# Optimization experiments

Hardware: AMD Instinct MI355X
Metric: run time of the kernel (lower is better)

Reference implementation:

```python
import jax, jax.numpy as jnp
import numpy as np

EMBED = 1024
HEADS = 16


def setup_inputs() -> dict:
    key = jax.random.key(0)
    ks = jax.random.split(key, 7)
    scale = 1.0 / np.sqrt(EMBED)
    x = jax.random.normal(ks[0], (4, 2048, EMBED), dtype=jnp.float32)
    Wq = jax.random.normal(ks[1], (EMBED, EMBED), dtype=jnp.float32) * scale
    bq = jax.random.normal(ks[2], (EMBED,), dtype=jnp.float32) * 0.01
    Wk = jax.random.normal(ks[3], (EMBED, EMBED), dtype=jnp.float32) * scale
    bk = jax.random.normal(ks[4], (EMBED,), dtype=jnp.float32) * 0.01
    Wv = jax.random.normal(ks[5], (EMBED, EMBED), dtype=jnp.float32) * scale
    bv = jax.random.normal(ks[6], (EMBED,), dtype=jnp.float32) * 0.01
    return {"x": x, "Wq": Wq, "bq": bq, "Wk": Wk, "bk": bk, "Wv": Wv, "bv": bv}


def reference(x, Wq, bq, Wk, bk, Wv, bv):
    b, s, n = x.shape
    h = HEADS
    d = n // h
    # torch nn.Linear: y = x @ W.T + b
    q = (jnp.einsum("bsn,mn->bsm", x, Wq) + bq).reshape(b, s, h, d).transpose(0, 2, 1, 3)
    k = (jnp.einsum("bsn,mn->bsm", x, Wk) + bk).reshape(b, s, h, d).transpose(0, 2, 1, 3)
    v = (jnp.einsum("bsn,mn->bsm", x, Wv) + bv).reshape(b, s, h, d).transpose(0, 2, 1, 3)
    # scores: [b, h, s_q, s_k]; fixed scale of 1/10 as in the source
    scores = jnp.einsum("bhqd,bhkd->bhqk", q, k) / 10.0
    # NOTE: softmax over dim=-2 (the QUERY axis), matching the source exactly
    attn = jax.nn.softmax(scores, axis=-2)
    out = jnp.einsum("bhqk,bhkd->bhqd", attn, v)
    return out.transpose(0, 2, 1, 3).reshape(b, s, n)
```

## Files before the change

### kernel.cpp

```cpp
#include <hip/hip_runtime.h>
#include <math.h>

#define SEQ    2048
#define EMBED  1024
#define HEADS  16
#define HDIM   64
#define BATCH  4
#define ROWS   (BATCH * SEQ)
#define BH     (BATCH * HEADS)

typedef _Float16 f16;
typedef __attribute__((ext_vector_type(8))) _Float16 f16x8;
typedef __attribute__((ext_vector_type(4))) _Float16 f16x4;
typedef __attribute__((ext_vector_type(4))) float    f32x4;

#define LOG2E_10 0.14426950408889634f

__device__ __forceinline__ float fast_exp2(float x) { return __builtin_amdgcn_exp2f(x); }

__device__ __forceinline__ void async16(void* l, const void* g) {
    __builtin_amdgcn_global_load_lds(
        (__attribute__((address_space(1))) void*)(uintptr_t)g,
        (__attribute__((address_space(3))) void*)(uint32_t)(uintptr_t)l,
        16, 0, 0);
}

__device__ __forceinline__ f32x4 mfma16(f16x8 a, f16x8 b, f32x4 c) {
    return __builtin_amdgcn_mfma_f32_16x16x32_f16(a, b, c, 0, 0, 0);
}
__device__ __forceinline__ f32x4 mfma16k16(f16x4 a, f16x4 b, f32x4 c) {
    return __builtin_amdgcn_mfma_f32_16x16x16f16(a, b, c, 0, 0, 0);
}

#define NX4 (ROWS * EMBED / 4)
#define NW4 (EMBED * EMBED / 4)
__global__ __launch_bounds__(256) void cvt_kernel(
    const float* __restrict__ x,
    const float* __restrict__ Wq, const float* __restrict__ Wk,
    const float* __restrict__ Wv,
    f16* __restrict__ xh, f16* __restrict__ Wh)
{
    int i = blockIdx.x * 256 + threadIdx.x;
    const float4* src; f16* dst; int j;
    if (i < NX4)              { src = (const float4*)x;  dst = xh;                j = i; }
    else if (i < NX4 + NW4)   { src = (const float4*)Wq; dst = Wh;                j = i - NX4; }
    else if (i < NX4 + 2*NW4) { src = (const float4*)Wk; dst = Wh + EMBED*EMBED;  j = i - NX4 - NW4; }
    else                      { src = (const float4*)Wv; dst = Wh + 2*EMBED*EMBED;j = i - NX4 - 2*NW4; }
    float4 v = src[j];
    f16x4 h;
    h[0] = (f16)v.x; h[1] = (f16)v.y; h[2] = (f16)v.z; h[3] = (f16)v.w;
    *(f16x4*)(dst + (size_t)j * 4) = h;
}

__global__ __launch_bounds__(256) void proj_kernel(
    const f16* __restrict__ A,
    const f16* __restrict__ W,
    const float* __restrict__ bq, const float* __restrict__ bk,
    const float* __restrict__ bv,
    f16* __restrict__ Qh, f16* __restrict__ Kh, f16* __restrict__ Vt)
{
    __shared__ f16 As[128 * 32];
    __shared__ f16 Bs[128 * 32];

    const int t = threadIdx.x, wv = t >> 6, lane = t & 63;
    const int lm = lane & 15, quad = lane >> 4;
    const int r0 = blockIdx.x * 128, c0 = blockIdx.y * 128;
    const int wm = wv & 1, wn = wv >> 1;

    const int srow = wv * 32 + (lane >> 2);
    const int sch  = (lane & 3) * 8;
    const f16* gA = A + (size_t)(r0 + srow) * EMBED + sch;
    const f16* gB = W + (size_t)(c0 + srow) * EMBED + sch;
    f16* lA = As + wv * 1024;
    f16* lB = Bs + wv * 1024;

    f32x4 acc[4][4];
#pragma unroll
    for (int i = 0; i < 4; ++i)
#pragma unroll
        for (int j = 0; j < 4; ++j) acc[i][j] = (f32x4){0.f, 0.f, 0.f, 0.f};

    for (int kk = 0; kk < EMBED; kk += 32) {
        __syncthreads();
        async16(lA,        gA + kk);
        async16(lA + 512,  gA + 16 * EMBED + kk);
        async16(lB,        gB + kk);
        async16(lB + 512,  gB + 16 * EMBED + kk);
        __syncthreads();

        f16x8 af[4], bf[4];
#pragma unroll
        for (int i = 0; i < 4; ++i)
            af[i] = *(const f16x8*)&As[(wm * 64 + i * 16 + lm) * 32 + quad * 8];
#pragma unroll
        for (int i = 0; i < 4; ++i)
            bf[i] = *(const f16x8*)&Bs[(wn * 64 + i * 16 + lm) * 32 + quad * 8];
#pragma unroll
        for (int mi = 0; mi < 4; ++mi)
#pragma unroll
            for (int ni = 0; ni < 4; ++ni)
                acc[mi][ni] = mfma16(af[mi], bf[ni], acc[mi][ni]);
    }

    const int z = c0 >> 10;
    const float* bias = (z == 0) ? bq : (z == 1) ? bk : bv;
    const float osc = (z == 0) ? LOG2E_10 : 1.0f;
#pragma unroll
    for (int ni = 0; ni < 4; ++ni) {
        int col = c0 + wn * 64 + ni * 16 + lm;
        int cz  = col & 1023;
        float bb = bias[cz];
        int h = cz >> 6, d = cz & 63;
#pragma unroll
        for (int mi = 0; mi < 4; ++mi) {
            int rbase = r0 + wm * 64 + mi * 16 + quad * 4;
            int b = rbase >> 11, s = rbase & 2047;
            if (z < 2) {
                f16* O = (z == 0) ? Qh : Kh;
                size_t base = ((size_t)(b * HEADS + h) * SEQ + s) * HDIM + d;
#pragma unroll
                for (int r = 0; r < 4; ++r)
                    O[base + (size_t)r * HDIM] = (f16)((acc[mi][ni][r] + bb) * osc);
            } else {
                f16x4 pk;
#pragma unroll
                for (int r = 0; r < 4; ++r) pk[r] = (f16)(acc[mi][ni][r] + bb);
                *(f16x4*)&Vt[((size_t)(b * HEADS + h) * HDIM + d) * SEQ + s] = pk;
            }
        }
    }
}

__device__ __forceinline__ void xcd_decode(int d, int& bh, int& x128) {
    int xcd  = d & 7;
    int r    = d >> 3;
    x128     = (r & 15) * 128;
    bh       = (r >> 4) * 8 + xcd;
}

__global__ __launch_bounds__(256) void stats_kernel(
    const f16* __restrict__ Qh, const f16* __restrict__ Kh,
    const f16* __restrict__ Vt, f16* __restrict__ Vt2)
{
    __shared__ f16 Ks[128 * 64];
    __shared__ f16 Qs[64 * 64];

    const int t = threadIdx.x, wv = t >> 6, lane = t & 63;
    const int lm = lane & 15, quad = lane >> 4;
    int bh, k0;
    xcd_decode(blockIdx.x, bh, k0);
    const int grow = lane >> 3;
    const int gsw  = ((lane & 7) ^ grow) * 8;
    const int rs   = lm & 7;
    const size_t base = (size_t)bh * SEQ * HDIM;

#pragma unroll
    for (int i = 0; i < 4; ++i) {
        int g = wv * 4 + i;
        async16(Ks + g * 512, Kh + base + (size_t)(k0 + g * 8 + grow) * HDIM + gsw);
    }
    __syncthreads();

    f16x8 kf[2][2];
#pragma unroll
    for (int ct = 0; ct < 2; ++ct)
#pragma unroll
        for (int ds = 0; ds < 2; ++ds)
            kf[ct][ds] = *(const f16x8*)&Ks[(wv * 32 + ct * 16 + lm) * 64
                                            + (((ds * 4 + quad) ^ rs) << 3)];

    float cs0 = 0.f, cs1 = 0.f;
    for (int q0 = 0; q0 < SEQ; q0 += 64) {
        __syncthreads();
#pragma unroll
        for (int i = 0; i < 2; ++i) {
            int g = wv * 2 + i;
            async16(Qs + g * 512, Qh + base + (size_t)(q0 + g * 8 + grow) * HDIM + gsw);
        }
        __syncthreads();
#pragma unroll
        for (int qt = 0; qt < 4; ++qt) {
            f16x8 a0 = *(const f16x8*)&Qs[(qt * 16 + lm) * 64 + ((quad ^ rs) << 3)];
            f16x8 a1 = *(const f16x8*)&Qs[(qt * 16 + lm) * 64 + (((4 + quad) ^ rs) << 3)];
            f32x4 c0v = (f32x4){0.f, 0.f, 0.f, 0.f};
            f32x4 c1v = (f32x4){0.f, 0.f, 0.f, 0.f};
            c0v = mfma16(a0, kf[0][0], c0v); c0v = mfma16(a1, kf[0][1], c0v);
            c1v = mfma16(a0, kf[1][0], c1v); c1v = mfma16(a1, kf[1][1], c1v);
#pragma unroll
            for (int r = 0; r < 4; ++r) {
                cs0 += fast_exp2(c0v[r]);
                cs1 += fast_exp2(c1v[r]);
            }
        }
    }
    cs0 += __shfl_xor(cs0, 16, 64); cs0 += __shfl_xor(cs0, 32, 64);
    cs1 += __shfl_xor(cs1, 16, 64); cs1 += __shfl_xor(cs1, 32, 64);

    __syncthreads();
    float* sc = (float*)Qs;
    if (quad == 0) {
        sc[wv * 32 + lm]      = 1024.0f / cs0;
        sc[wv * 32 + 16 + lm] = 1024.0f / cs1;
    }
    __syncthreads();
    const int row = t >> 2, cb = (t & 3) * 32;
    const f16* src = Vt  + base + (size_t)row * SEQ + k0 + cb;
    f16*       dst = Vt2 + base + (size_t)row * SEQ + k0 + cb;
#pragma unroll
    for (int c = 0; c < 4; ++c) {
        f16x8 v = *(const f16x8*)(src + c * 8);
        f16x8 o;
#pragma unroll
        for (int j = 0; j < 8; ++j)
            o[j] = (f16)((float)v[j] * sc[cb + c * 8 + j]);
        *(f16x8*)(dst + c * 8) = o;
    }
}

__global__ __launch_bounds__(256) void out_kernel(
    const f16* __restrict__ Qh, const f16* __restrict__ Kh,
    const f16* __restrict__ Vt2, float* __restrict__ out)
{
    __shared__ f16 L[16384];

    const int t = threadIdx.x, wv = t >> 6, lane = t & 63;
    const int lm = lane & 15, quad = lane >> 4;
    const int wq = wv >> 1, wk = wv & 1;
    int bh, q0;
    xcd_decode(blockIdx.x, bh, q0);
    const int b = bh >> 4, h = bh & 15;
    const int grow = lane >> 3;
    const int gsw  = ((lane & 7) ^ grow) * 8;
    const int rs   = lm & 7;
    const size_t base = (size_t)bh * SEQ * HDIM;

    f16* Ks = L;
    f16* Vs = L + 8192;

    f16x8 qa[4][2];
#pragma unroll
    for (int qt = 0; qt < 4; ++qt)
#pragma unroll
        for (int ds = 0; ds < 2; ++ds)
            qa[qt][ds] = *(const f16x8*)(Qh + base
                          + (size_t)(q0 + wq * 64 + qt * 16 + lm) * HDIM
                          + ds * 32 + quad * 8);

#pragma unroll
    for (int i = 0; i < 2; ++i) {
        int g = wv * 2 + i;
        async16(Ks + g * 512, Kh  + base + (size_t)(g * 8 + grow) * HDIM + gsw);
        async16(Vs + g * 512, Vt2 + base + (size_t)(g * 8 + grow) * SEQ + gsw);
    }
    __syncthreads();

    f32x4 oacc[4][4];
#pragma unroll
    for (int i = 0; i < 4; ++i)
#pragma unroll
        for (int j = 0; j < 4; ++j) oacc[i][j] = (f32x4){0.f, 0.f, 0.f, 0.f};

    for (int it = 0; it < SEQ / 64; ++it) {
        const int cur = it & 1;
        if (it + 1 < SEQ / 64) {
            const int nxt = cur ^ 1, k0n = (it + 1) * 64;
#pragma unroll
            for (int i = 0; i < 2; ++i) {
                int g = wv * 2 + i;
                async16(Ks + nxt * 4096 + g * 512,
                        Kh + base + (size_t)(k0n + g * 8 + grow) * HDIM + gsw);
                async16(Vs + nxt * 4096 + g * 512,
                        Vt2 + base + (size_t)(g * 8 + grow) * SEQ + k0n + gsw);
            }
        }
        const f16* Kb = Ks + cur * 4096;
        const f16* Vb = Vs + cur * 4096;

#pragma unroll
        for (int ct = 0; ct < 2; ++ct) {
            const int kb = wk * 32 + ct * 16;
            f16x8 kf0 = *(const f16x8*)&Kb[(kb + lm) * 64 + ((quad ^ rs) << 3)];
            f16x8 kf1 = *(const f16x8*)&Kb[(kb + lm) * 64 + (((4 + quad) ^ rs) << 3)];
            const int vch = ((wk * 4 + ct * 2 + (quad >> 1)) ^ rs);
            f16x4 vb[4];
#pragma unroll
            for (int dt = 0; dt < 4; ++dt)
                vb[dt] = *(const f16x4*)&Vb[(dt * 16 + lm) * 64 + vch * 8 + (quad & 1) * 4];
#pragma unroll
            for (int qt = 0; qt < 4; ++qt) {
                f32x4 s4 = (f32x4){0.f, 0.f, 0.f, 0.f};
                s4 = mfma16(kf0, qa[qt][0], s4);
                s4 = mfma16(kf1, qa[qt][1], s4);
                f16x4 pa;
#pragma unroll
                for (int r = 0; r < 4; ++r)
                    pa[r] = (f16)fast_exp2(s4[r]);
#pragma unroll
                for (int dt = 0; dt < 4; ++dt)
                    oacc[qt][dt] = mfma16k16(pa, vb[dt], oacc[qt][dt]);
            }
        }
        __syncthreads();
    }

    float* red = (float*)L;
    if (wk == 1) {
#pragma unroll
        for (int qt = 0; qt < 4; ++qt)
#pragma unroll
            for (int dt = 0; dt < 4; ++dt)
#pragma unroll
                for (int r = 0; r < 4; ++r)
                    red[wq * 4096 + (qt * 16 + quad * 4 + r) * 64 + dt * 16 + lm]
                        = oacc[qt][dt][r];
    }
    __syncthreads();
    if (wk == 0) {
        const float inv1024 = 1.0f / 1024.0f;
#pragma unroll
        for (int qt = 0; qt < 4; ++qt)
#pragma unroll
            for (int dt = 0; dt < 4; ++dt) {
                int col = h * HDIM + dt * 16 + lm;
#pragma unroll
                for (int r = 0; r < 4; ++r) {
                    int ql = qt * 16 + quad * 4 + r;
                    int s  = q0 + wq * 64 + ql;
                    float v = oacc[qt][dt][r]
                            + red[wq * 4096 + ql * 64 + dt * 16 + lm];
                    out[((size_t)b * SEQ + s) * EMBED + col] = v * inv1024;
                }
            }
    }
}

extern "C" void kernel_launch(void* const* d_in, const int* in_sizes, int n_in,
                              void* d_out, int out_size, void* d_ws, size_t ws_size,
                              hipStream_t stream) {
    const float* x  = (const float*)d_in[0];
    const float* Wq = (const float*)d_in[1];
    const float* bq = (const float*)d_in[2];
    const float* Wk = (const float*)d_in[3];
    const float* bk = (const float*)d_in[4];
    const float* Wv = (const float*)d_in[5];
    const float* bv = (const float*)d_in[6];
    float* out = (float*)d_out;

    f16* xh = (f16*)d_ws;
    f16* Wh = xh + (size_t)ROWS * EMBED;
    f16* Qh = Wh + (size_t)3 * EMBED * EMBED;
    f16* Kh = Qh + (size_t)BH * SEQ * HDIM;
    f16* Vt = Kh + (size_t)BH * SEQ * HDIM;
    f16* Vt2 = xh;

    cvt_kernel<<<(NX4 + 3 * NW4) / 256, 256, 0, stream>>>(x, Wq, Wk, Wv, xh, Wh);
    proj_kernel<<<dim3(ROWS / 128, 3 * EMBED / 128), 256, 0, stream>>>(
        xh, Wh, bq, bk, bv, Qh, Kh, Vt);
    stats_kernel<<<dim3(SEQ / 128 * BH), 256, 0, stream>>>(Qh, Kh, Vt, Vt2);
    out_kernel<<<dim3(SEQ / 128 * BH), 256, 0, stream>>>(Qh, Kh, Vt2, out);
}
```

Before: 323.0 us.

## Prefetch two tiles ahead with explicit vmcnt waits in stats and out kernels

Both the stats and attention-output kernels now issue async global-to-LDS loads two tiles ahead into a double buffer. They replace __syncthreads with targeted s_waitcnt vmcnt/lgkmcnt waits plus raw barriers, so loads can stay in flight across iterations. The out kernel also stages its Q tile through LDS with the swizzled layout instead of direct strided global loads. The aim is to hide global memory latency behind MFMA and exp work, at the cost of fragile hand-counted wait values that assume a fixed number of outstanding loads per thread.

```diff
diff --git a/kernel.cpp b/kernel.cpp
--- a/kernel.cpp
+++ b/kernel.cpp
@@ -8,6 +8,7 @@
 #define BATCH  4
 #define ROWS   (BATCH * SEQ)
 #define BH     (BATCH * HEADS)
+#define NT     (SEQ / 64)
 
 typedef _Float16 f16;
 typedef __attribute__((ext_vector_type(8))) _Float16 f16x8;
@@ -17,6 +18,12 @@
 #define LOG2E_10 0.14426950408889634f
 
 __device__ __forceinline__ float fast_exp2(float x) { return __builtin_amdgcn_exp2f(x); }
+
+#define WAIT_VM0() asm volatile("s_waitcnt vmcnt(0)" ::: "memory")
+#define WAIT_VM2() asm volatile("s_waitcnt vmcnt(2)" ::: "memory")
+#define WAIT_VM4() asm volatile("s_waitcnt vmcnt(4)" ::: "memory")
+#define WAIT_LGKM0() asm volatile("s_waitcnt lgkmcnt(0)" ::: "memory")
+#define BAR() __builtin_amdgcn_s_barrier()
 
 __device__ __forceinline__ void async16(void* l, const void* g) {
     __builtin_amdgcn_global_load_lds(
@@ -143,7 +150,7 @@
     const f16* __restrict__ Vt, f16* __restrict__ Vt2)
 {
     __shared__ f16 Ks[128 * 64];
-    __shared__ f16 Qs[64 * 64];
+    __shared__ f16 Qs[2 * 64 * 64];
 
     const int t = threadIdx.x, wv = t >> 6, lane = t & 63;
     const int lm = lane & 15, quad = lane >> 4;
@@ -159,7 +166,16 @@
         int g = wv * 4 + i;
         async16(Ks + g * 512, Kh + base + (size_t)(k0 + g * 8 + grow) * HDIM + gsw);
     }
-    __syncthreads();
+#pragma unroll
+    for (int bi = 0; bi < 2; ++bi)
+#pragma unroll
+        for (int i = 0; i < 2; ++i) {
+            int g = wv * 2 + i;
+            async16(Qs + bi * 4096 + g * 512,
+                    Qh + base + (size_t)(bi * 64 + g * 8 + grow) * HDIM + gsw);
+        }
+    WAIT_VM4();
+    BAR();
 
     f16x8 kf[2][2];
 #pragma unroll
@@ -170,18 +186,15 @@
                                             + (((ds * 4 + quad) ^ rs) << 3)];
 
     float cs0 = 0.f, cs1 = 0.f;
-    for (int q0 = 0; q0 < SEQ; q0 += 64) {
-        __syncthreads();
-#pragma unroll
-        for (int i = 0; i < 2; ++i) {
-            int g = wv * 2 + i;
-            async16(Qs + g * 512, Qh + base + (size_t)(q0 + g * 8 + grow) * HDIM + gsw);
-        }
-        __syncthreads();
+    for (int it = 0; it < NT; ++it) {
+        const int cur = it & 1;
+        if (it == NT - 1) WAIT_VM0(); else WAIT_VM2();
+        BAR();
+        const f16* Qb = Qs + cur * 4096;
 #pragma unroll
         for (int qt = 0; qt < 4; ++qt) {
-            f16x8 a0 = *(const f16x8*)&Qs[(qt * 16 + lm) * 64 + ((quad ^ rs) << 3)];
-            f16x8 a1 = *(const f16x8*)&Qs[(qt * 16 + lm) * 64 + (((4 + quad) ^ rs) << 3)];
+            f16x8 a0 = *(const f16x8*)&Qb[(qt * 16 + lm) * 64 + ((quad ^ rs) << 3)];
+            f16x8 a1 = *(const f16x8*)&Qb[(qt * 16 + lm) * 64 + (((4 + quad) ^ rs) << 3)];
             f32x4 c0v = (f32x4){0.f, 0.f, 0.f, 0.f};
             f32x4 c1v = (f32x4){0.f, 0.f, 0.f, 0.f};
             c0v = mfma16(a0, kf[0][0], c0v); c0v = mfma16(a1, kf[0][1], c0v);
@@ -192,11 +205,21 @@
                 cs1 += fast_exp2(c1v[r]);
             }
         }
+        WAIT_LGKM0();
+        BAR();
+        if (it + 2 < NT) {
+            const int qn = (it + 2) * 64;
+#pragma unroll
+            for (int i = 0; i < 2; ++i) {
+                int g = wv * 2 + i;
+                async16(Qs + cur * 4096 + g * 512,
+                        Qh + base + (size_t)(qn + g * 8 + grow) * HDIM + gsw);
+            }
+        }
     }
     cs0 += __shfl_xor(cs0, 16, 64); cs0 += __shfl_xor(cs0, 32, 64);
     cs1 += __shfl_xor(cs1, 16, 64); cs1 += __shfl_xor(cs1, 32, 64);
 
-    __syncthreads();
     float* sc = (float*)Qs;
     if (quad == 0) {
         sc[wv * 32 + lm]      = 1024.0f / cs0;
@@ -234,25 +257,32 @@
     const int rs   = lm & 7;
     const size_t base = (size_t)bh * SEQ * HDIM;
 
-    f16* Ks = L;
-    f16* Vs = L + 8192;
-
+#pragma unroll
+    for (int i = 0; i < 4; ++i) {
+        int g = wv * 4 + i;
+        async16(L + g * 512, Qh + base + (size_t)(q0 + g * 8 + grow) * HDIM + gsw);
+    }
+    WAIT_VM0();
+    BAR();
     f16x8 qa[4][2];
 #pragma unroll
     for (int qt = 0; qt < 4; ++qt)
 #pragma unroll
         for (int ds = 0; ds < 2; ++ds)
-            qa[qt][ds] = *(const f16x8*)(Qh + base
-                          + (size_t)(q0 + wq * 64 + qt * 16 + lm) * HDIM
-                          + ds * 32 + quad * 8);
-
-#pragma unroll
-    for (int i = 0; i < 2; ++i) {
-        int g = wv * 2 + i;
-        async16(Ks + g * 512, Kh  + base + (size_t)(g * 8 + grow) * HDIM + gsw);
-        async16(Vs + g * 512, Vt2 + base + (size_t)(g * 8 + grow) * SEQ + gsw);
-    }
-    __syncthreads();
+            qa[qt][ds] = *(const f16x8*)&L[(wq * 64 + qt * 16 + lm) * 64
+                                           + (((ds * 4 + quad) ^ rs) << 3)];
+    WAIT_LGKM0();
+    BAR();
+#pragma unroll
+    for (int bi = 0; bi < 2; ++bi)
+#pragma unroll
+        for (int i = 0; i < 2; ++i) {
+            int g = wv * 2 + i;
+            async16(L + bi * 4096 + g * 512,
+                    Kh + base + (size_t)(bi * 64 + g * 8 + grow) * HDIM + gsw);
+            async16(L + 8192 + bi * 4096 + g * 512,
+                    Vt2 + base + (size_t)(g * 8 + grow) * SEQ + bi * 64 + gsw);
+        }
 
     f32x4 oacc[4][4];
 #pragma unroll
@@ -260,21 +290,12 @@
 #pragma unroll
         for (int j = 0; j < 4; ++j) oacc[i][j] = (f32x4){0.f, 0.f, 0.f, 0.f};
 
-    for (int it = 0; it < SEQ / 64; ++it) {
+    for (int it = 0; it < NT; ++it) {
         const int cur = it & 1;
-        if (it + 1 < SEQ / 64) {
-            const int nxt = cur ^ 1, k0n = (it + 1) * 64;
-#pragma unroll
-            for (int i = 0; i < 2; ++i) {
-                int g = wv * 2 + i;
-                async16(Ks + nxt * 4096 + g * 512,
-                        Kh + base + (size_t)(k0n + g * 8 + grow) * HDIM + gsw);
-                async16(Vs + nxt * 4096 + g * 512,
-                        Vt2 + base + (size_t)(g * 8 + grow) * SEQ + k0n + gsw);
-            }
-        }
-        const f16* Kb = Ks + cur * 4096;
-        const f16* Vb = Vs + cur * 4096;
+        if (it == NT - 1) WAIT_VM0(); else WAIT_VM4();
+        BAR();
+        const f16* Kb = L + cur * 4096;
+        const f16* Vb = L + 8192 + cur * 4096;
 
 #pragma unroll
         for (int ct = 0; ct < 2; ++ct) {
@@ -300,7 +321,19 @@
                     oacc[qt][dt] = mfma16k16(pa, vb[dt], oacc[qt][dt]);
             }
         }
-        __syncthreads();
+        WAIT_LGKM0();
+        BAR();
+        if (it + 2 < NT) {
+            const int kn = (it + 2) * 64;
+#pragma unroll
+            for (int i = 0; i < 2; ++i) {
+                int g = wv * 2 + i;
+                async16(L + cur * 4096 + g * 512,
+                        Kh + base + (size_t)(kn + g * 8 + grow) * HDIM + gsw);
+                async16(L + 8192 + cur * 4096 + g * 512,
+                        Vt2 + base + (size_t)(g * 8 + grow) * SEQ + kn + gsw);
+            }
+        }
     }
 
     float* red = (float*)L;
```

Result: faster. 307.0 us, median of 2 (-5.0%).
